# Kernel optimization log

Hardware: AMD Instinct MI355X
Metric: run time of the kernel (lower is better)

Reference implementation:

```python
import jax, jax.numpy as jnp
import numpy as np

L = 16384      # sequence length
CH = 512       # input channels
S = 128        # SSM state dim


def setup_inputs() -> dict:
    key = jax.random.key(0)
    kx, kb, kc, kdt = jax.random.split(key, 4)
    x = jax.random.normal(kx, (L, CH), dtype=jnp.float32)
    # logA init matches flax param init: log(1 + arange(state_dim))
    logA = jnp.log(1.0 + jnp.arange(S, dtype=jnp.float32))
    # Dense (no bias) kernels, lecun-normal-ish scale 1/sqrt(fan_in)
    scale = 1.0 / np.sqrt(CH)
    WB = jax.random.normal(kb, (CH, S), dtype=jnp.float32) * scale
    WC = jax.random.normal(kc, (CH, S), dtype=jnp.float32) * scale
    Wdt = jax.random.normal(kdt, (CH, 1), dtype=jnp.float32) * scale
    bdt = jnp.zeros((1,), dtype=jnp.float32)
    return {"x": x, "logA": logA, "WB": WB, "WC": WC, "Wdt": Wdt, "bdt": bdt}


def reference(x, logA, WB, WC, Wdt, bdt):
    A = -jnp.exp(logA)                      # (S,)
    B = x @ WB                              # (L, S)
    C = x @ WC                              # (L, S)
    dt = jax.nn.softplus(x @ Wdt + bdt)     # (L, 1), learned since dt=None
    Abar = jnp.exp(A * dt)                  # (L, S) discretized transition
    Bbar = (Abar - 1.0) * B / A             # (L, S) discretized input term

    def scan_fn(el1, el2):
        (A1, B1), (A2, B2) = el1, el2
        return (A1 * A2, A1 * B2)           # faithful to source (non-standard combine)

    _, AkB = jax.lax.associative_scan(scan_fn, (Abar, Bbar))  # over axis 0 (L)
    return jnp.einsum('ls,ls,lc->lc', C, AkB, x)              # (L, CH)
```

## Files before the change

kernel.cpp:

```cpp
#include <hip/hip_runtime.h>
#include <math.h>

#define L_SEQ  16384
#define CHN    512
#define S_DIM  128
#define NPRE   2048
#define E_CUT  104.0f

static __device__ __forceinline__ float softplus_f(float z) {
    return (z > 20.f) ? z : log1pf(expf(z));
}

__global__ __launch_bounds__(256) void k_zero(float4* __restrict__ out)
{
    const size_t total = (size_t)L_SEQ * CHN / 4;
    size_t i = (size_t)blockIdx.x * 256 + threadIdx.x;
    const size_t step = (size_t)gridDim.x * 256;
    for (; i < total; i += step)
        out[i] = make_float4(0.f, 0.f, 0.f, 0.f);
}

__global__ __launch_bounds__(256) void k_dt(const float* __restrict__ x,
                                            const float* __restrict__ Wdt,
                                            const float* __restrict__ bdt,
                                            float* __restrict__ dt)
{
    const int wave = threadIdx.x >> 6;
    const int lane = threadIdx.x & 63;
    const int row  = blockIdx.x * 4 + wave;

    const float4* xr = (const float4*)(x + (size_t)row * CHN);
    const float4* w4 = (const float4*)Wdt;

    float acc = 0.f;
#pragma unroll
    for (int i = 0; i < 2; ++i) {
        float4 xv = xr[lane + 64 * i];
        float4 wv = w4[lane + 64 * i];
        acc = fmaf(xv.x, wv.x, acc);
        acc = fmaf(xv.y, wv.y, acc);
        acc = fmaf(xv.z, wv.z, acc);
        acc = fmaf(xv.w, wv.w, acc);
    }
#pragma unroll
    for (int off = 32; off; off >>= 1) acc += __shfl_down(acc, off);

    if (lane == 0) dt[row] = softplus_f(acc + bdt[0]);
}

__global__ __launch_bounds__(1024) void k_scan(const float* __restrict__ dt,
                                               float* __restrict__ E,
                                               int*   __restrict__ n_p,
                                               int*   __restrict__ need_p,
                                               float* __restrict__ total_p)
{
    __shared__ float sums[1024];
    __shared__ int   cnt_s;
    const int t = threadIdx.x;

    float v0 = dt[2 * t], v1 = dt[2 * t + 1];
    float tot = v0 + v1;
    sums[t] = tot;
    if (t == 0) cnt_s = 0;
    __syncthreads();

    float s = tot;
    for (int off = 1; off < 1024; off <<= 1) {
        float add = (t >= off) ? sums[t - off] : 0.f;
        __syncthreads();
        s += add;
        sums[t] = s;
        __syncthreads();
    }
    const float excl = (t > 0) ? sums[t - 1] : 0.f;

    E[2 * t]     = excl;
    E[2 * t + 1] = excl + v0;

    int cnt = (excl < E_CUT) + (excl + v0 < E_CUT);
#pragma unroll
    for (int off = 32; off; off >>= 1) cnt += __shfl_down(cnt, off);
    if ((t & 63) == 0) atomicAdd(&cnt_s, cnt);
    __syncthreads();

    if (t == 0) {
        n_p[0]     = cnt_s;
        need_p[0]  = (cnt_s == NPRE) ? 1 : 0;
        total_p[0] = sums[1023];
    }
}

__global__ __launch_bounds__(64) void k_fallback(const float* __restrict__ x,
                                                 const float* __restrict__ Wdt,
                                                 const float* __restrict__ bdt,
                                                 float* __restrict__ dt,
                                                 float* __restrict__ E,
                                                 int*   __restrict__ n_p,
                                                 const int*   __restrict__ need_p,
                                                 const float* __restrict__ total_p)
{
    if (need_p[0] == 0) return;
    const int lane = threadIdx.x;
    float running = total_p[0];
    int n = NPRE;
    for (int l = NPRE; l < L_SEQ && running < E_CUT; ++l) {
        const float4* xr = (const float4*)(x + (size_t)l * CHN);
        const float4* w4 = (const float4*)Wdt;
        float acc = 0.f;
#pragma unroll
        for (int i = 0; i < 2; ++i) {
            float4 xv = xr[lane + 64 * i];
            float4 wv = w4[lane + 64 * i];
            acc = fmaf(xv.x, wv.x, acc); acc = fmaf(xv.y, wv.y, acc);
            acc = fmaf(xv.z, wv.z, acc); acc = fmaf(xv.w, wv.w, acc);
        }
#pragma unroll
        for (int off = 32; off; off >>= 1) acc += __shfl_down(acc, off);
        float d = softplus_f(__shfl(acc, 0) + bdt[0]);
        if (lane == 0) { E[l] = running; dt[l] = d; }
        running += d;
        ++n;
    }
    if (lane == 0) n_p[0] = n;
}

__global__ __launch_bounds__(256) void k_active(const float* __restrict__ x,
                                                const float* __restrict__ logA,
                                                const float* __restrict__ WB,
                                                const float* __restrict__ WC,
                                                const float* __restrict__ dt,
                                                const float* __restrict__ E,
                                                const int* __restrict__ n_p,
                                                float* __restrict__ out)
{
    const int n = n_p[0];
    const int t  = threadIdx.x;
    const int g  = t >> 5;
    const int s4 = t & 31;

    __shared__ float  xs[CHN];
    __shared__ float4 redB[8][32];
    __shared__ float4 redC[8][32];
    __shared__ float  scal;

    const float4* wb = (const float4*)WB;
    const float4* wc = (const float4*)WC;

    for (int l = blockIdx.x; l < n; l += gridDim.x) {
        ((float2*)xs)[t] = ((const float2*)(x + (size_t)l * CHN))[t];
        __syncthreads();

        float4 aB = make_float4(0.f, 0.f, 0.f, 0.f);
        float4 aC = make_float4(0.f, 0.f, 0.f, 0.f);
#pragma unroll 8
        for (int c = g; c < CHN; c += 8) {
            const float  xc = xs[c];
            const float4 b  = wb[c * 32 + s4];
            const float4 cc = wc[c * 32 + s4];
            aB.x = fmaf(xc, b.x,  aB.x);  aB.y = fmaf(xc, b.y,  aB.y);
            aB.z = fmaf(xc, b.z,  aB.z);  aB.w = fmaf(xc, b.w,  aB.w);
            aC.x = fmaf(xc, cc.x, aC.x);  aC.y = fmaf(xc, cc.y, aC.y);
            aC.z = fmaf(xc, cc.z, aC.z);  aC.w = fmaf(xc, cc.w, aC.w);
        }
        redB[g][s4] = aB;
        redC[g][s4] = aC;
        __syncthreads();

        if (t < 32) {
            float4 B = redB[0][t], C = redC[0][t];
#pragma unroll
            for (int k = 1; k < 8; ++k) {
                float4 b = redB[k][t], c = redC[k][t];
                B.x += b.x; B.y += b.y; B.z += b.z; B.w += b.w;
                C.x += c.x; C.y += c.y; C.z += c.z; C.w += c.w;
            }
            const float  e   = E[l];
            const float  dtl = dt[l];
            const float4 la  = ((const float4*)logA)[t];

            float con = 0.f;
            {
                float a = -expf(la.x);
                con = fmaf(C.x * expf(a * e), expm1f(a * dtl) * B.x / a, con);
                a = -expf(la.y);
                con = fmaf(C.y * expf(a * e), expm1f(a * dtl) * B.y / a, con);
                a = -expf(la.z);
                con = fmaf(C.z * expf(a * e), expm1f(a * dtl) * B.z / a, con);
                a = -expf(la.w);
                con = fmaf(C.w * expf(a * e), expm1f(a * dtl) * B.w / a, con);
            }
#pragma unroll
            for (int off = 16; off; off >>= 1) con += __shfl_down(con, off);
            if (t == 0) scal = con;
        }
        __syncthreads();

        const float  sc = scal;
        const float2 xv = ((float2*)xs)[t];
        ((float2*)(out + (size_t)l * CHN))[t] = make_float2(sc * xv.x, sc * xv.y);
        __syncthreads();
    }
}

extern "C" void kernel_launch(void* const* d_in, const int* in_sizes, int n_in,
                              void* d_out, int out_size, void* d_ws, size_t ws_size,
                              hipStream_t stream)
{
    const float* x    = (const float*)d_in[0];
    const float* logA = (const float*)d_in[1];
    const float* WB   = (const float*)d_in[2];
    const float* WC   = (const float*)d_in[3];
    const float* Wdt  = (const float*)d_in[4];
    const float* bdt  = (const float*)d_in[5];
    float* out = (float*)d_out;

    float* dt      = (float*)d_ws;
    float* E       = dt + L_SEQ;
    int*   n_p     = (int*)(E + L_SEQ);
    int*   need_p  = n_p + 1;
    float* total_p = (float*)(n_p + 2);

    k_zero    <<<2048,     256,  0, stream>>>((float4*)out);
    k_dt      <<<NPRE / 4, 256,  0, stream>>>(x, Wdt, bdt, dt);
    k_scan    <<<1,        1024, 0, stream>>>(dt, E, n_p, need_p, total_p);
    k_fallback<<<1,        64,   0, stream>>>(x, Wdt, bdt, dt, E, n_p, need_p, total_p);
    k_active  <<<256,      256,  0, stream>>>(x, logA, WB, WC, dt, E, n_p, out);
}
```

Measured before the change: 39.35 us.

## Merge scan with fallback, fold output zeroing into active kernel

Fuses the single-block prefix scan and the sequential fallback into one single-wave kernel that uses register-local scans and wave shuffles instead of a 1024-thread shared-memory scan. The separate zero-fill kernel is removed, and the output kernel now writes zeros for rows past the cutoff, launched with 2048 blocks. NPRE is halved to shrink the precompute. Together these cut two launches and redundant writes to rows that get overwritten, at the cost of a longer serial fallback if the cutoff lies beyond the precomputed rows.

```diff
diff --git a/kernel.cpp b/kernel.cpp
--- a/kernel.cpp
+++ b/kernel.cpp
@@ -4,20 +4,11 @@
 #define L_SEQ  16384
 #define CHN    512
 #define S_DIM  128
-#define NPRE   2048
+#define NPRE   1024
 #define E_CUT  104.0f
 
 static __device__ __forceinline__ float softplus_f(float z) {
     return (z > 20.f) ? z : log1pf(expf(z));
-}
-
-__global__ __launch_bounds__(256) void k_zero(float4* __restrict__ out)
-{
-    const size_t total = (size_t)L_SEQ * CHN / 4;
-    size_t i = (size_t)blockIdx.x * 256 + threadIdx.x;
-    const size_t step = (size_t)gridDim.x * 256;
-    for (; i < total; i += step)
-        out[i] = make_float4(0.f, 0.f, 0.f, 0.f);
 }
 
 __global__ __launch_bounds__(256) void k_dt(const float* __restrict__ x,
@@ -48,92 +39,84 @@
     if (lane == 0) dt[row] = softplus_f(acc + bdt[0]);
 }
 
-__global__ __launch_bounds__(1024) void k_scan(const float* __restrict__ dt,
-                                               float* __restrict__ E,
-                                               int*   __restrict__ n_p,
-                                               int*   __restrict__ need_p,
-                                               float* __restrict__ total_p)
-{
-    __shared__ float sums[1024];
-    __shared__ int   cnt_s;
-    const int t = threadIdx.x;
-
-    float v0 = dt[2 * t], v1 = dt[2 * t + 1];
-    float tot = v0 + v1;
-    sums[t] = tot;
-    if (t == 0) cnt_s = 0;
-    __syncthreads();
-
-    float s = tot;
-    for (int off = 1; off < 1024; off <<= 1) {
-        float add = (t >= off) ? sums[t - off] : 0.f;
-        __syncthreads();
-        s += add;
-        sums[t] = s;
-        __syncthreads();
-    }
-    const float excl = (t > 0) ? sums[t - 1] : 0.f;
-
-    E[2 * t]     = excl;
-    E[2 * t + 1] = excl + v0;
-
-    int cnt = (excl < E_CUT) + (excl + v0 < E_CUT);
+__global__ __launch_bounds__(64) void k_scan_fb(const float* __restrict__ x,
+                                                const float* __restrict__ Wdt,
+                                                const float* __restrict__ bdt,
+                                                float* __restrict__ dt,
+                                                float* __restrict__ E,
+                                                int*   __restrict__ n_p)
+{
+    const int lane = threadIdx.x;
+    const int PER  = NPRE / 64;
+
+    float v[PER], ex[PER];
+    const float4* dt4 = (const float4*)dt;
+#pragma unroll
+    for (int i = 0; i < PER / 4; ++i) {
+        float4 q = dt4[lane * (PER / 4) + i];
+        v[4*i+0] = q.x; v[4*i+1] = q.y; v[4*i+2] = q.z; v[4*i+3] = q.w;
+    }
+
+    float run = 0.f;
+#pragma unroll
+    for (int i = 0; i < PER; ++i) { ex[i] = run; run += v[i]; }
+
+    float incl = run;
+#pragma unroll
+    for (int off = 1; off < 64; off <<= 1) {
+        float o = __shfl_up(incl, off);
+        if (lane >= off) incl += o;
+    }
+    const float excl  = incl - run;
+    const float total = __shfl(incl, 63);
+
+    float4* E4 = (float4*)E;
+#pragma unroll
+    for (int i = 0; i < PER / 4; ++i)
+        E4[lane * (PER / 4) + i] = make_float4(excl + ex[4*i],   excl + ex[4*i+1],
+                                               excl + ex[4*i+2], excl + ex[4*i+3]);
+
+    int cnt = 0;
+#pragma unroll
+    for (int i = 0; i < PER; ++i) cnt += (excl + ex[i] < E_CUT) ? 1 : 0;
 #pragma unroll
     for (int off = 32; off; off >>= 1) cnt += __shfl_down(cnt, off);
-    if ((t & 63) == 0) atomicAdd(&cnt_s, cnt);
-    __syncthreads();
-
-    if (t == 0) {
-        n_p[0]     = cnt_s;
-        need_p[0]  = (cnt_s == NPRE) ? 1 : 0;
-        total_p[0] = sums[1023];
-    }
-}
-
-__global__ __launch_bounds__(64) void k_fallback(const float* __restrict__ x,
-                                                 const float* __restrict__ Wdt,
-                                                 const float* __restrict__ bdt,
-                                                 float* __restrict__ dt,
-                                                 float* __restrict__ E,
-                                                 int*   __restrict__ n_p,
-                                                 const int*   __restrict__ need_p,
-                                                 const float* __restrict__ total_p)
-{
-    if (need_p[0] == 0) return;
-    const int lane = threadIdx.x;
-    float running = total_p[0];
-    int n = NPRE;
-    for (int l = NPRE; l < L_SEQ && running < E_CUT; ++l) {
-        const float4* xr = (const float4*)(x + (size_t)l * CHN);
-        const float4* w4 = (const float4*)Wdt;
-        float acc = 0.f;
-#pragma unroll
-        for (int i = 0; i < 2; ++i) {
-            float4 xv = xr[lane + 64 * i];
-            float4 wv = w4[lane + 64 * i];
-            acc = fmaf(xv.x, wv.x, acc); acc = fmaf(xv.y, wv.y, acc);
-            acc = fmaf(xv.z, wv.z, acc); acc = fmaf(xv.w, wv.w, acc);
-        }
-#pragma unroll
-        for (int off = 32; off; off >>= 1) acc += __shfl_down(acc, off);
-        float d = softplus_f(__shfl(acc, 0) + bdt[0]);
-        if (lane == 0) { E[l] = running; dt[l] = d; }
-        running += d;
-        ++n;
+    int n = __shfl(cnt, 0);
+
+    if (n == NPRE) {
+        float running = total;
+        for (int l = NPRE; l < L_SEQ && running < E_CUT; ++l) {
+            const float4* xr = (const float4*)(x + (size_t)l * CHN);
+            const float4* w4 = (const float4*)Wdt;
+            float acc = 0.f;
+#pragma unroll
+            for (int i = 0; i < 2; ++i) {
+                float4 xv = xr[lane + 64 * i];
+                float4 wv = w4[lane + 64 * i];
+                acc = fmaf(xv.x, wv.x, acc); acc = fmaf(xv.y, wv.y, acc);
+                acc = fmaf(xv.z, wv.z, acc); acc = fmaf(xv.w, wv.w, acc);
+            }
+#pragma unroll
+            for (int off = 32; off; off >>= 1) acc += __shfl_down(acc, off);
+            float d = softplus_f(__shfl(acc, 0) + bdt[0]);
+            if (lane == 0) { E[l] = running; dt[l] = d; }
+            running += d;
+            ++n;
+        }
     }
     if (lane == 0) n_p[0] = n;
 }
 
-__global__ __launch_bounds__(256) void k_active(const float* __restrict__ x,
-                                                const float* __restrict__ logA,
-                                                const float* __restrict__ WB,
-                                                const float* __restrict__ WC,
-                                                const float* __restrict__ dt,
-                                                const float* __restrict__ E,
-                                                const int* __restrict__ n_p,
-                                                float* __restrict__ out)
-{
-    const int n = n_p[0];
+__global__ __launch_bounds__(256) void k_out(const float* __restrict__ x,
+                                             const float* __restrict__ logA,
+                                             const float* __restrict__ WB,
+                                             const float* __restrict__ WC,
+                                             const float* __restrict__ dt,
+                                             const float* __restrict__ E,
+                                             const int* __restrict__ n_p,
+                                             float* __restrict__ out)
+{
+    const int n  = n_p[0];
     const int t  = threadIdx.x;
     const int g  = t >> 5;
     const int s4 = t & 31;
@@ -146,7 +129,14 @@
     const float4* wb = (const float4*)WB;
     const float4* wc = (const float4*)WC;
 
-    for (int l = blockIdx.x; l < n; l += gridDim.x) {
+    for (int l = blockIdx.x; l < L_SEQ; l += gridDim.x) {
+        float* orow = out + (size_t)l * CHN;
+
+        if (l >= n) {
+            ((float2*)orow)[t] = make_float2(0.f, 0.f);
+            continue;
+        }
+
         ((float2*)xs)[t] = ((const float2*)(x + (size_t)l * CHN))[t];
         __syncthreads();
 
@@ -197,7 +187,7 @@
 
         const float  sc = scal;
         const float2 xv = ((float2*)xs)[t];
-        ((float2*)(out + (size_t)l * CHN))[t] = make_float2(sc * xv.x, sc * xv.y);
+        ((float2*)orow)[t] = make_float2(sc * xv.x, sc * xv.y);
         __syncthreads();
     }
 }
@@ -214,15 +204,11 @@
     const float* bdt  = (const float*)d_in[5];
     float* out = (float*)d_out;
 
-    float* dt      = (float*)d_ws;
-    float* E       = dt + L_SEQ;
-    int*   n_p     = (int*)(E + L_SEQ);
-    int*   need_p  = n_p + 1;
-    float* total_p = (float*)(n_p + 2);
-
-    k_zero    <<<2048,     256,  0, stream>>>((float4*)out);
-    k_dt      <<<NPRE / 4, 256,  0, stream>>>(x, Wdt, bdt, dt);
-    k_scan    <<<1,        1024, 0, stream>>>(dt, E, n_p, need_p, total_p);
-    k_fallback<<<1,        64,   0, stream>>>(x, Wdt, bdt, dt, E, n_p, need_p, total_p);
-    k_active  <<<256,      256,  0, stream>>>(x, logA, WB, WC, dt, E, n_p, out);
-}
+    float* dt  = (float*)d_ws;
+    float* E   = dt + L_SEQ;
+    int*   n_p = (int*)(E + L_SEQ);
+
+    k_dt     <<<NPRE / 4, 256, 0, stream>>>(x, Wdt, bdt, dt);
+    k_scan_fb<<<1,        64,  0, stream>>>(x, Wdt, bdt, dt, E, n_p);
+    k_out    <<<2048,     256, 0, stream>>>(x, logA, WB, WC, dt, E, n_p, out);
+}
```

After: 35.20 us. 10.6% less time.
